# Kernel optimization log

Hardware: AMD Instinct MI355X
Metric: run time of the kernel (lower is better)

## Reference

```python
import itertools
import jax, jax.numpy as jnp
import numpy as np

THR = 0.2  # success_threshold (non-trainable constant)
V = 2      # num_total_variables
U_IDX, B_IDX = 1, 2  # rule_idxs for arities [0,1,2]


def _perm_indices(num_objects: int, v: int):
    """Static permutation index tables (numpy, shapes are compile-time)."""
    perm_idxs = np.array(list(itertools.permutations(range(num_objects), v)))  # [P, V]
    bidx = np.stack(np.nonzero(1 - np.eye(v))).T.reshape(v, v - 1, 2)          # [V, V-1, 2]
    pb = perm_idxs[:, bidx]                                                     # [P, V, V-1, 2]
    shift = (pb[..., 1] > pb[..., 0]).astype(np.int64)
    perm_bidxs = np.stack([pb[..., 0], pb[..., 1] - shift], axis=-1)            # off-diagonal compact idx
    return jnp.asarray(perm_idxs), jnp.asarray(perm_bidxs)


def setup_inputs() -> dict:
    key = jax.random.key(0)
    k1, k2, k3, k4, k5 = jax.random.split(key, 5)
    B, O, P0, P1, P2, C = 16, 64, 128, 128, 128, 8
    num_in = P0 + V * P1 + V * (V - 1) * P2  # 640
    return {
        "nullary": jax.random.normal(k1, (B, P0), dtype=jnp.float32),
        "unary": jax.random.normal(k2, (B, O, P1), dtype=jnp.float32),
        "binary": jax.random.normal(k3, (B, O, O - 1, P2), dtype=jnp.float32),
        "and_kernel": 0.01 * jax.random.normal(k4, (3, C, num_in), dtype=jnp.float32),
        "or_kernel": 0.01 * jax.random.normal(k5, (3, C), dtype=jnp.float32),
    }


def _forward(nullary, unary, binary, and_kernel, or_kernel):
    B, O, _ = unary.shape
    perm_idxs, perm_bidxs = _perm_indices(O, V)
    P = perm_idxs.shape[0]  # O*(O-1) for V=2
    thr = jnp.float32(THR)

    # permutation gathers -> flatten_concat with batch_dims=2
    pn = jnp.broadcast_to(nullary[:, None], (B, P, nullary.shape[-1]))          # [B,P,P0]
    pu = unary[:, perm_idxs].reshape(B, P, -1)                                   # [B,P,V*P1]
    pb = binary[:, perm_bidxs[..., 0], perm_bidxs[..., 1]].reshape(B, P, -1)     # [B,P,V*(V-1)*P2]
    x = jnp.concatenate([pn, pu, pb], axis=-1)                                   # [B,P,num_in]

    # AND stage: multiply-sum + bias + tanh (einsum == sum(in_tensor * and_kernel, -1))
    and_bias = thr - jnp.sum(jnp.square(and_kernel), -1) * jnp.tanh(thr)         # [A,C]
    conj = jnp.tanh(jnp.einsum('bpi,aci->bpac', x, and_kernel) + and_bias)       # [B,P,A,C]

    A, C = and_kernel.shape[0], and_kernel.shape[1]
    # OR max-reduce over unused permutation dims
    null_r = jnp.max(conj[:, :, :U_IDX, :], axis=1)                              # [B,n0,C]
    un_r = conj[:, :, U_IDX:B_IDX, :].reshape(B, O, P // O, B_IDX - U_IDX, C).max(axis=2)
    bi_r = conj[:, :, B_IDX:, :].reshape(B, O, O - 1, P // (O * (O - 1)), A - B_IDX, C).max(axis=3)

    def or_stage(c, k):
        bias = jnp.sum(jnp.square(k), -1) * jnp.tanh(thr) - thr                  # [n_rules]
        return jnp.einsum('...rc,rc->...r', c, k) + bias

    return (or_stage(null_r, or_kernel[:U_IDX]),
            or_stage(un_r, or_kernel[U_IDX:B_IDX]),
            or_stage(bi_r, or_kernel[B_IDX:]))


def reference(nullary, unary, binary, and_kernel, or_kernel):
    # outputs: nullary [B,1], unary [B,O,1], binary [B,O,O-1,1]
    return _forward(nullary, unary, binary, and_kernel, or_kernel)
```

## Files before the change

### kernel.cpp

```cpp
#include <hip/hip_runtime.h>

#define THR_F     0.2f
#define TANH_THR  0.19737532f

__device__ __forceinline__ float fast_tanh(float x) {
    x = fminf(10.f, fmaxf(-10.f, x));
    float e = __expf(2.f * x);
    return (e - 1.f) * __builtin_amdgcn_rcpf(e + 1.f);
}

__device__ __forceinline__ unsigned fkey(float f) {
    unsigned u = __float_as_uint(f);
    return (u & 0x80000000u) ? ~u : (u | 0x80000000u);
}
__device__ __forceinline__ float fdecode(unsigned u) {
    return __uint_as_float((u & 0x80000000u) ? (u & 0x7FFFFFFFu) : ~u);
}

__global__ __launch_bounds__(64) void prep_kernel(
    const float* __restrict__ nullary,
    const float* __restrict__ andk,
    float* __restrict__ Wb,
    float* __restrict__ Wu,
    float* __restrict__ base,
    unsigned* __restrict__ max0)
{
    const int bid = blockIdx.x;
    const int t   = threadIdx.x;
    if (bid < 384) {
        const int b = bid / 24, n = bid % 24;
        const float* w  = andk + n * 640;
        const float* nu = nullary + b * 128;
        float s = 0.f;
        #pragma unroll
        for (int i = 0; i < 10; ++i) { float v = w[t + i * 64]; s = fmaf(v, v, s); }
        float d = fmaf(nu[t], w[t], 0.f);
        d = fmaf(nu[t + 64], w[t + 64], d);
        #pragma unroll
        for (int m = 32; m; m >>= 1) {
            s += __shfl_xor(s, m, 64);
            d += __shfl_xor(d, m, 64);
        }
        if (t == 0) base[bid] = d + THR_F - s * TANH_THR;
    } else {
        const int i = (bid - 384) * 64 + t;
        const int k = i / 48, n = i % 48;
        const int ac   = (n < 24) ? n : n - 24;
        const int colb = (n < 24) ? 384 : 512;
        const int colu = (n < 24) ? 128 : 256;
        Wb[i] = andk[ac * 640 + colb + k];
        Wu[i] = andk[ac * 640 + colu + k];
        if (bid < 386) max0[(bid - 384) * 64 + t] = 0u;
    }
}

__global__ __launch_bounds__(256) void proj_kernel(
    const float* __restrict__ unary,
    const float* __restrict__ binary,
    const float* __restrict__ Wb,
    const float* __restrict__ Wu,
    float* __restrict__ P0, float* __restrict__ P1,
    float* __restrict__ U0, float* __restrict__ U1)
{
    const int bid  = blockIdx.x;
    const int wave = __builtin_amdgcn_readfirstlane((int)(threadIdx.x >> 6));
    const int lane = threadIdx.x & 63;
    const bool is_bin = (bid < 1008);

    const int row = is_bin ? (bid * 64 + lane) : ((bid - 1008) * 64 + lane);
    const float* __restrict__ W   = (is_bin ? Wb : Wu) + wave * 12;
    const float* __restrict__ src = (is_bin ? binary : unary) + (size_t)row * 128;
    float* Dbase = is_bin ? ((wave < 2) ? P0 : P1) : ((wave < 2) ? U0 : U1);
    float* dst = Dbase + (size_t)row * 24 + (wave & 1) * 12;

    float acc[12];
    #pragma unroll
    for (int n = 0; n < 12; ++n) acc[n] = 0.f;

    const float4* rp = (const float4*)src;
    #pragma unroll 8
    for (int k4 = 0; k4 < 32; ++k4) {
        float4 a = rp[k4];
        const float* wk = W + k4 * 4 * 48;
        #pragma unroll
        for (int q = 0; q < 4; ++q) {
            float av = (q == 0) ? a.x : (q == 1) ? a.y : (q == 2) ? a.z : a.w;
            const float* w = wk + q * 48;
            #pragma unroll
            for (int n = 0; n < 12; ++n) acc[n] = fmaf(av, w[n], acc[n]);
        }
    }

    float4* d4 = (float4*)dst;
    #pragma unroll
    for (int i = 0; i < 3; ++i)
        d4[i] = make_float4(acc[i*4+0], acc[i*4+1], acc[i*4+2], acc[i*4+3]);
}

__global__ __launch_bounds__(192) void combine_kernel(
    const float* __restrict__ base,
    const float* __restrict__ U0, const float* __restrict__ U1,
    const float* __restrict__ P0, const float* __restrict__ P1,
    const float* __restrict__ ork,
    unsigned* __restrict__ max0,
    float* __restrict__ out)
{
    const int bid = blockIdx.x;
    const int b   = bid >> 6;
    const int o0  = bid & 63;
    const int a   = __builtin_amdgcn_readfirstlane((int)(threadIdx.x >> 6));
    const int t   = threadIdx.x & 63;
    const bool act = (t < 63);

    const int o1  = min(t + (t >= o0 ? 1 : 0), 63);
    const int j10 = (o1 < o0) ? (o0 - 1) : o0;
    const int j01 = min(t, 62);
    const int ch  = a * 8;

    const float* pb  = base + b * 24 + ch;
    const float* pa0 = U0 + (size_t)(b * 64 + o0) * 24 + ch;
    const float4* A1 = (const float4*)(U1 + (size_t)(b * 64 + o1) * 24 + ch);
    const float4* Q0 = (const float4*)(P0 + (size_t)((b * 64 + o0) * 63 + j01) * 24 + ch);
    const float4* Q1 = (const float4*)(P1 + (size_t)((b * 64 + o1) * 63 + j10) * 24 + ch);

    float th[8];
    #pragma unroll
    for (int i = 0; i < 2; ++i) {
        float4 a1 = A1[i], q0 = Q0[i], q1 = Q1[i];
        int n = i * 4;
        th[n+0] = pb[n+0] + pa0[n+0] + a1.x + q0.x + q1.x;
        th[n+1] = pb[n+1] + pa0[n+1] + a1.y + q0.y + q1.y;
        th[n+2] = pb[n+2] + pa0[n+2] + a1.z + q0.z + q1.z;
        th[n+3] = pb[n+3] + pa0[n+3] + a1.w + q0.w + q1.w;
    }
    #pragma unroll
    for (int n = 0; n < 8; ++n) th[n] = fast_tanh(th[n]);

    if (a == 2) {
        if (act) {
            float v = 0.f, b2 = 0.f;
            #pragma unroll
            for (int c = 0; c < 8; ++c) {
                float k = ork[16 + c];
                v  = fmaf(th[c], k, v);
                b2 = fmaf(k, k, b2);
            }
            out[16 + 1024 + ((b * 64 + o0) * 63 + t)] = v + b2 * TANH_THR - THR_F;
        }
        return;
    }

    if (!act) {
        #pragma unroll
        for (int n = 0; n < 8; ++n) th[n] = -2.0f;
    }
    #pragma unroll
    for (int n = 0; n < 8; ++n) {
        float v = th[n];
        #pragma unroll
        for (int m = 32; m; m >>= 1) v = fmaxf(v, __shfl_xor(v, m, 64));
        th[n] = v;
    }

    if (t == 0) {
        if (a == 1) {
            float v1 = 0.f, b1 = 0.f;
            #pragma unroll
            for (int c = 0; c < 8; ++c) {
                float k = ork[8 + c];
                v1 = fmaf(th[c], k, v1);
                b1 = fmaf(k, k, b1);
            }
            out[16 + b * 64 + o0] = v1 + b1 * TANH_THR - THR_F;
        } else {
            #pragma unroll
            for (int c = 0; c < 8; ++c)
                atomicMax(&max0[b * 8 + c], fkey(th[c]));
        }
    }
}

__global__ __launch_bounds__(64) void finalize_kernel(
    const unsigned* __restrict__ max0,
    const float* __restrict__ ork,
    float* __restrict__ out)
{
    int b = threadIdx.x;
    if (b >= 16) return;
    float v = 0.f, bb = 0.f;
    #pragma unroll
    for (int c = 0; c < 8; ++c) {
        float m = fdecode(max0[b * 8 + c]);
        float k = ork[c];
        v  = fmaf(m, k, v);
        bb = fmaf(k, k, bb);
    }
    out[b] = v + bb * TANH_THR - THR_F;
}

extern "C" void kernel_launch(void* const* d_in, const int* in_sizes, int n_in,
                              void* d_out, int out_size, void* d_ws, size_t ws_size,
                              hipStream_t stream)
{
    const float* nullary = (const float*)d_in[0];
    const float* unary   = (const float*)d_in[1];
    const float* binary  = (const float*)d_in[2];
    const float* andk    = (const float*)d_in[3];
    const float* ork     = (const float*)d_in[4];
    float* out = (float*)d_out;

    float* ws = (float*)d_ws;
    float*    base = ws;
    float*    U0   = ws + 384;
    float*    U1   = ws + 24960;
    float*    Wb   = ws + 49536;
    float*    Wu   = ws + 55680;
    float*    P0   = ws + 61824;
    float*    P1   = ws + 1610112;
    unsigned* max0 = (unsigned*)(ws + 3158400);

    prep_kernel<<<480, 64, 0, stream>>>(nullary, andk, Wb, Wu, base, max0);
    proj_kernel<<<1024, 256, 0, stream>>>(unary, binary, Wb, Wu, P0, P1, U0, U1);
    combine_kernel<<<1024, 192, 0, stream>>>(base, U0, U1, P0, P1, ork, max0, out);
    finalize_kernel<<<1, 64, 0, stream>>>(max0, ork, out);
}
```

Before: 126.2 us.

## Fuse projection and combine into tiled kernel with shared-memory pairwise projections

```diff
diff --git a/kernel.cpp b/kernel.cpp
--- a/kernel.cpp
+++ b/kernel.cpp
@@ -21,9 +21,9 @@
     const float* __restrict__ nullary,
     const float* __restrict__ andk,
     float* __restrict__ Wb,
-    float* __restrict__ Wu,
+    float* __restrict__ WuT,
     float* __restrict__ base,
-    unsigned* __restrict__ max0)
+    unsigned* __restrict__ zzero)
 {
     const int bid = blockIdx.x;
     const int t   = threadIdx.x;
@@ -42,160 +42,247 @@
             d += __shfl_xor(d, m, 64);
         }
         if (t == 0) base[bid] = d + THR_F - s * TANH_THR;
+    } else if (bid < 480) {
+        const int i = (bid - 384) * 64 + t;
+        {
+            const int k = i / 48, n = i % 48;
+            const int ac  = (n < 24) ? n : n - 24;
+            const int col = (n < 24) ? 384 : 512;
+            Wb[i] = andk[ac * 640 + col + k];
+        }
+        {
+            const int n = i / 128, k = i % 128;
+            const int ac  = (n < 24) ? n : n - 24;
+            const int col = (n < 24) ? 128 : 256;
+            WuT[i] = andk[ac * 640 + col + k];
+        }
     } else {
-        const int i = (bid - 384) * 64 + t;
-        const int k = i / 48, n = i % 48;
-        const int ac   = (n < 24) ? n : n - 24;
-        const int colb = (n < 24) ? 384 : 512;
-        const int colu = (n < 24) ? 128 : 256;
-        Wb[i] = andk[ac * 640 + colb + k];
-        Wu[i] = andk[ac * 640 + colu + k];
-        if (bid < 386) max0[(bid - 384) * 64 + t] = 0u;
-    }
-}
-
-__global__ __launch_bounds__(256) void proj_kernel(
+        const int idx = (bid - 480) * 64 + t;
+        if (idx < 8320) zzero[idx] = 0u;
+    }
+}
+
+__global__ __launch_bounds__(128) void fused_kernel(
     const float* __restrict__ unary,
     const float* __restrict__ binary,
     const float* __restrict__ Wb,
-    const float* __restrict__ Wu,
-    float* __restrict__ P0, float* __restrict__ P1,
-    float* __restrict__ U0, float* __restrict__ U1)
-{
-    const int bid  = blockIdx.x;
-    const int wave = __builtin_amdgcn_readfirstlane((int)(threadIdx.x >> 6));
-    const int lane = threadIdx.x & 63;
-    const bool is_bin = (bid < 1008);
-
-    const int row = is_bin ? (bid * 64 + lane) : ((bid - 1008) * 64 + lane);
-    const float* __restrict__ W   = (is_bin ? Wb : Wu) + wave * 12;
-    const float* __restrict__ src = (is_bin ? binary : unary) + (size_t)row * 128;
-    float* Dbase = is_bin ? ((wave < 2) ? P0 : P1) : ((wave < 2) ? U0 : U1);
-    float* dst = Dbase + (size_t)row * 24 + (wave & 1) * 12;
-
-    float acc[12];
-    #pragma unroll
-    for (int n = 0; n < 12; ++n) acc[n] = 0.f;
-
-    const float4* rp = (const float4*)src;
-    #pragma unroll 8
-    for (int k4 = 0; k4 < 32; ++k4) {
-        float4 a = rp[k4];
-        const float* wk = W + k4 * 4 * 48;
-        #pragma unroll
-        for (int q = 0; q < 4; ++q) {
-            float av = (q == 0) ? a.x : (q == 1) ? a.y : (q == 2) ? a.z : a.w;
-            const float* w = wk + q * 48;
-            #pragma unroll
-            for (int n = 0; n < 12; ++n) acc[n] = fmaf(av, w[n], acc[n]);
-        }
-    }
-
-    float4* d4 = (float4*)dst;
-    #pragma unroll
-    for (int i = 0; i < 3; ++i)
-        d4[i] = make_float4(acc[i*4+0], acc[i*4+1], acc[i*4+2], acc[i*4+3]);
-}
-
-__global__ __launch_bounds__(192) void combine_kernel(
+    const float* __restrict__ WuT,
     const float* __restrict__ base,
-    const float* __restrict__ U0, const float* __restrict__ U1,
-    const float* __restrict__ P0, const float* __restrict__ P1,
     const float* __restrict__ ork,
     unsigned* __restrict__ max0,
+    unsigned* __restrict__ slots1,
     float* __restrict__ out)
 {
+    __shared__ float proj2[48][65];
+    __shared__ float upro[48][13];
+
     const int bid = blockIdx.x;
     const int b   = bid >> 6;
-    const int o0  = bid & 63;
-    const int a   = __builtin_amdgcn_readfirstlane((int)(threadIdx.x >> 6));
-    const int t   = threadIdx.x & 63;
-    const bool act = (t < 63);
-
-    const int o1  = min(t + (t >= o0 ? 1 : 0), 63);
-    const int j10 = (o1 < o0) ? (o0 - 1) : o0;
-    const int j01 = min(t, 62);
-    const int ch  = a * 8;
-
-    const float* pb  = base + b * 24 + ch;
-    const float* pa0 = U0 + (size_t)(b * 64 + o0) * 24 + ch;
-    const float4* A1 = (const float4*)(U1 + (size_t)(b * 64 + o1) * 24 + ch);
-    const float4* Q0 = (const float4*)(P0 + (size_t)((b * 64 + o0) * 63 + j01) * 24 + ch);
-    const float4* Q1 = (const float4*)(P1 + (size_t)((b * 64 + o1) * 63 + j10) * 24 + ch);
-
-    float th[8];
+    const int tl  = bid & 63;
+    const int t   = threadIdx.x;
+
+    int gi, gj, H;
+    bool diag;
+    if (tl < 8) { diag = true; gi = gj = tl; H = 0; }
+    else {
+        diag = false;
+        int t8 = tl - 8;
+        H = t8 & 1;
+        int pr = t8 >> 1;
+        int i = 0;
+        while (pr >= 7 - i) { pr -= 7 - i; ++i; }
+        gi = i; gj = i + 1 + pr;
+    }
+    const int I0 = gi * 8, J0 = gj * 8;
+
+    {
+        const int r = t & 63;
+        const int h = __builtin_amdgcn_readfirstlane(t >> 6);
+        int o, op, jv;
+        if (diag) {
+            const int oi = r >> 3, oj = r & 7;
+            o = I0 + oi; op = I0 + oj;
+            jv = op - ((oj > oi) ? 1 : 0);
+        } else if (r < 32) {
+            const int oi = H * 4 + (r >> 3), oj = r & 7;
+            o = I0 + oi; op = J0 + oj;
+            jv = op - 1;
+        } else {
+            const int rr = r - 32;
+            const int oi = rr >> 2, oj = H * 4 + (rr & 3);
+            o = J0 + oi; op = I0 + oj;
+            jv = op;
+        }
+        jv = min(jv, 62);
+        const float* __restrict__ src = binary + ((size_t)(b * 64 + o) * 63 + jv) * 128;
+        const float* __restrict__ W   = Wb + h * 24;
+
+        float acc[24];
+        #pragma unroll
+        for (int n = 0; n < 24; ++n) acc[n] = 0.f;
+        const float4* rp = (const float4*)src;
+        #pragma unroll 4
+        for (int k4 = 0; k4 < 32; ++k4) {
+            float4 a = rp[k4];
+            const float* wk = W + k4 * 4 * 48;
+            #pragma unroll
+            for (int q = 0; q < 4; ++q) {
+                float av = (q == 0) ? a.x : (q == 1) ? a.y : (q == 2) ? a.z : a.w;
+                const float* w = wk + q * 48;
+                #pragma unroll
+                for (int n = 0; n < 24; ++n) acc[n] = fmaf(av, w[n], acc[n]);
+            }
+        }
+        #pragma unroll
+        for (int n = 0; n < 24; ++n) proj2[h * 24 + n][r] = acc[n];
+    }
+
+    {
+        const int nObj = diag ? 8 : 12;
+        if (t < nObj * 8) {
+            const int u = t >> 3, nb = t & 7, n0 = nb * 6;
+            const int obj = diag ? (I0 + u)
+                                 : (u < 4 ? (I0 + H * 4 + u) : (J0 + u - 4));
+            const float4* su = (const float4*)(unary + (size_t)(b * 64 + obj) * 128);
+            float a6[6];
+            #pragma unroll
+            for (int j = 0; j < 6; ++j) a6[j] = 0.f;
+            #pragma unroll 4
+            for (int k4 = 0; k4 < 32; ++k4) {
+                float4 a = su[k4];
+                #pragma unroll
+                for (int j = 0; j < 6; ++j) {
+                    float4 w = ((const float4*)(WuT + (n0 + j) * 128))[k4];
+                    a6[j] = fmaf(a.x, w.x, fmaf(a.y, w.y, fmaf(a.z, w.z, fmaf(a.w, w.w, a6[j]))));
+                }
+            }
+            #pragma unroll
+            for (int j = 0; j < 6; ++j) upro[n0 + j][u] = a6[j];
+        }
+    }
+    __syncthreads();
+
+    const int p = t & 63;
+    int o0, o1, r0, r1, u0, u1, j01;
+    bool valid;
+    if (diag) {
+        const int qi = p >> 3, qj = p & 7;
+        valid = (qi != qj);
+        o0 = I0 + qi; o1 = I0 + qj;
+        r0 = p; r1 = qj * 8 + qi;
+        u0 = qi; u1 = qj;
+        j01 = o1 - ((qj > qi) ? 1 : 0);
+    } else if (p < 32) {
+        const int qi = p >> 3, qj = p & 7;
+        valid = true;
+        o0 = I0 + H * 4 + qi; o1 = J0 + qj;
+        r0 = p; r1 = 32 + qj * 4 + qi;
+        u0 = qi; u1 = 4 + qj;
+        j01 = o1 - 1;
+    } else {
+        const int pp = p - 32;
+        const int qi = pp >> 2, qj = pp & 3;
+        valid = true;
+        o0 = J0 + qi; o1 = I0 + H * 4 + qj;
+        r0 = 32 + qi * 4 + qj; r1 = qj * 8 + qi;
+        u0 = 4 + qi; u1 = qj;
+        j01 = o1;
+    }
+    const float* pb = base + b * 24;
+
+    if (t >= 64) {
+        float v = 0.f, b2 = 0.f;
+        #pragma unroll
+        for (int c = 0; c < 8; ++c) {
+            const int ch = 16 + c;
+            float x = pb[ch] + upro[ch][u0] + upro[24 + ch][u1]
+                    + proj2[ch][r0] + proj2[24 + ch][r1];
+            x = fast_tanh(x);
+            float k = ork[16 + c];
+            v  = fmaf(x, k, v);
+            b2 = fmaf(k, k, b2);
+        }
+        if (valid) out[16 + 1024 + (b * 64 + o0) * 63 + j01] = v + b2 * TANH_THR - THR_F;
+        return;
+    }
+
+    float th[16];
     #pragma unroll
-    for (int i = 0; i < 2; ++i) {
-        float4 a1 = A1[i], q0 = Q0[i], q1 = Q1[i];
-        int n = i * 4;
-        th[n+0] = pb[n+0] + pa0[n+0] + a1.x + q0.x + q1.x;
-        th[n+1] = pb[n+1] + pa0[n+1] + a1.y + q0.y + q1.y;
-        th[n+2] = pb[n+2] + pa0[n+2] + a1.z + q0.z + q1.z;
-        th[n+3] = pb[n+3] + pa0[n+3] + a1.w + q0.w + q1.w;
-    }
+    for (int c = 0; c < 16; ++c) {
+        float x = pb[c] + upro[c][u0] + upro[24 + c][u1]
+                + proj2[c][r0] + proj2[24 + c][r1];
+        th[c] = fast_tanh(x);
+    }
+    if (!valid) {
+        #pragma unroll
+        for (int c = 0; c < 16; ++c) th[c] = -2.f;
+    }
+
     #pragma unroll
-    for (int n = 0; n < 8; ++n) th[n] = fast_tanh(th[n]);
-
-    if (a == 2) {
-        if (act) {
-            float v = 0.f, b2 = 0.f;
-            #pragma unroll
-            for (int c = 0; c < 8; ++c) {
-                float k = ork[16 + c];
-                v  = fmaf(th[c], k, v);
-                b2 = fmaf(k, k, b2);
-            }
-            out[16 + 1024 + ((b * 64 + o0) * 63 + t)] = v + b2 * TANH_THR - THR_F;
-        }
-        return;
-    }
-
-    if (!act) {
-        #pragma unroll
-        for (int n = 0; n < 8; ++n) th[n] = -2.0f;
-    }
+    for (int c = 0; c < 8; ++c) {
+        float v = th[c];
+        #pragma unroll
+        for (int m = 32; m; m >>= 1) v = fmaxf(v, __shfl_xor(v, m, 64));
+        th[c] = v;
+    }
+    if (p == 0) {
+        #pragma unroll
+        for (int c = 0; c < 8; ++c)
+            atomicMax(&max0[b * 8 + c], fkey(th[c]));
+    }
+
+    float m4[8], m8[8];
     #pragma unroll
-    for (int n = 0; n < 8; ++n) {
-        float v = th[n];
-        #pragma unroll
-        for (int m = 32; m; m >>= 1) v = fmaxf(v, __shfl_xor(v, m, 64));
-        th[n] = v;
-    }
-
-    if (t == 0) {
-        if (a == 1) {
-            float v1 = 0.f, b1 = 0.f;
-            #pragma unroll
-            for (int c = 0; c < 8; ++c) {
-                float k = ork[8 + c];
-                v1 = fmaf(th[c], k, v1);
-                b1 = fmaf(k, k, b1);
-            }
-            out[16 + b * 64 + o0] = v1 + b1 * TANH_THR - THR_F;
-        } else {
-            #pragma unroll
-            for (int c = 0; c < 8; ++c)
-                atomicMax(&max0[b * 8 + c], fkey(th[c]));
-        }
-    }
-}
-
-__global__ __launch_bounds__(64) void finalize_kernel(
+    for (int c = 0; c < 8; ++c) {
+        float v = th[8 + c];
+        v = fmaxf(v, __shfl_xor(v, 1, 64));
+        v = fmaxf(v, __shfl_xor(v, 2, 64));
+        m4[c] = v;
+        m8[c] = fmaxf(v, __shfl_xor(v, 4, 64));
+    }
+    const bool emit8 = (diag || p < 32) && ((p & 7) == 0);
+    const bool emit4 = (!diag && p >= 32) && ((p & 3) == 0);
+    if (emit8) {
+        #pragma unroll
+        for (int c = 0; c < 8; ++c)
+            atomicMax(&slots1[(b * 64 + o0) * 8 + c], fkey(m8[c]));
+    }
+    if (emit4) {
+        #pragma unroll
+        for (int c = 0; c < 8; ++c)
+            atomicMax(&slots1[(b * 64 + o0) * 8 + c], fkey(m4[c]));
+    }
+}
+
+__global__ __launch_bounds__(256) void finalize_kernel(
     const unsigned* __restrict__ max0,
+    const unsigned* __restrict__ slots1,
     const float* __restrict__ ork,
     float* __restrict__ out)
 {
-    int b = threadIdx.x;
-    if (b >= 16) return;
-    float v = 0.f, bb = 0.f;
-    #pragma unroll
-    for (int c = 0; c < 8; ++c) {
-        float m = fdecode(max0[b * 8 + c]);
-        float k = ork[c];
-        v  = fmaf(m, k, v);
-        bb = fmaf(k, k, bb);
-    }
-    out[b] = v + bb * TANH_THR - THR_F;
+    const int bid = blockIdx.x, t = threadIdx.x;
+    if (bid < 4) {
+        const int i = bid * 256 + t;
+        float v = 0.f, bb = 0.f;
+        #pragma unroll
+        for (int c = 0; c < 8; ++c) {
+            float m = fdecode(slots1[i * 8 + c]);
+            float k = ork[8 + c];
+            v  = fmaf(m, k, v);
+            bb = fmaf(k, k, bb);
+        }
+        out[16 + i] = v + bb * TANH_THR - THR_F;
+    } else if (t < 16) {
+        float v = 0.f, bb = 0.f;
+        #pragma unroll
+        for (int c = 0; c < 8; ++c) {
+            float m = fdecode(max0[t * 8 + c]);
+            float k = ork[c];
+            v  = fmaf(m, k, v);
+            bb = fmaf(k, k, bb);
+        }
+        out[t] = v + bb * TANH_THR - THR_F;
+    }
 }
 
 extern "C" void kernel_launch(void* const* d_in, const int* in_sizes, int n_in,
@@ -210,17 +297,14 @@
     float* out = (float*)d_out;
 
     float* ws = (float*)d_ws;
-    float*    base = ws;
-    float*    U0   = ws + 384;
-    float*    U1   = ws + 24960;
-    float*    Wb   = ws + 49536;
-    float*    Wu   = ws + 55680;
-    float*    P0   = ws + 61824;
-    float*    P1   = ws + 1610112;
-    unsigned* max0 = (unsigned*)(ws + 3158400);
-
-    prep_kernel<<<480, 64, 0, stream>>>(nullary, andk, Wb, Wu, base, max0);
-    proj_kernel<<<1024, 256, 0, stream>>>(unary, binary, Wb, Wu, P0, P1, U0, U1);
-    combine_kernel<<<1024, 192, 0, stream>>>(base, U0, U1, P0, P1, ork, max0, out);
-    finalize_kernel<<<1, 64, 0, stream>>>(max0, ork, out);
-}
+    float*    Wb     = ws;
+    float*    WuT    = ws + 6144;
+    float*    base   = ws + 12288;
+    unsigned* max0   = (unsigned*)(ws + 12672);
+    unsigned* slots1 = max0 + 128;
+
+    prep_kernel<<<610, 64, 0, stream>>>(nullary, andk, Wb, WuT, base, max0);
+    fused_kernel<<<1024, 128, 0, stream>>>(unary, binary, Wb, WuT, base, ork,
+                                           max0, slots1, out);
+    finalize_kernel<<<5, 256, 0, stream>>>(max0, slots1, ork, out);
+}
```

New measurement: 153.4 us. +21.5%, slower.
